# Performance work log

Measured on AMD Instinct MI355X. Metric: run time of the kernel, lower is better.

## Reference

```python
import jax, jax.numpy as jnp
import numpy as np

MASK_PROPORTION = 0.5
NEG_BIG = -99999999.0


def setup_inputs() -> dict:
    key = jax.random.key(0)
    k_x, k_w1, k_b1, k_w2, k_b2 = jax.random.split(key, 5)
    B, T, D, H = 32, 4096, 1024, 256
    x = jax.random.normal(k_x, (B, T, D), dtype=jnp.float32)
    s1 = 1.0 / np.sqrt(D)
    s2 = 1.0 / np.sqrt(H)
    W1 = jax.random.uniform(k_w1, (D, H), minval=-s1, maxval=s1, dtype=jnp.float32)
    b1 = jax.random.uniform(k_b1, (H,), minval=-s1, maxval=s1, dtype=jnp.float32)
    W2 = jax.random.uniform(k_w2, (H, 1), minval=-s2, maxval=s2, dtype=jnp.float32)
    b2 = jax.random.uniform(k_b2, (1,), minval=-s2, maxval=s2, dtype=jnp.float32)
    return {"x": x, "W1": W1, "b1": b1, "W2": W2, "b2": b2}


def reference(x, W1, b1, W2, b2):
    # e: [B, T, 1] attention scores from small MLP
    h = jnp.tanh(jnp.einsum("btd,dh->bth", x, W1) + b1)
    e = jnp.einsum("bth,ho->bto", h, W2) + b2  # [B, T, 1]

    T = e.shape[1]
    threshold_index = int(T * MASK_PROPORTION)
    sorted_e = jnp.sort(e, axis=1)
    threshold_value = sorted_e[:, threshold_index]          # [B, 1]
    # mask: +1 where e < threshold (kept), NEG_BIG where e >= threshold
    mask = jnp.where(e >= threshold_value[:, None, :], NEG_BIG, 1.0)
    e = e + mask
    beta = jax.nn.softmax(e, axis=1)                        # [B, T, 1]
    # bmm(beta^T, x) -> [B, 1, D], permute -> [B, D, 1], unsqueeze -> [B, D, 1, 1]
    out = jnp.einsum("bto,btd->bd", beta, x)
    return out[:, :, None, None]
```

## Files before the change

kernel.cpp:

```cpp
#include <hip/hip_runtime.h>
#include <hip/hip_bf16.h>
#include <math.h>

#define B_   32
#define T_   4096
#define D_   1024
#define H_   256
#define KTH  2048
#define NC   16
#define TC   (T_/NC)
#define BM   128
#define BKE  32
#define NTE  (D_/BKE)
#define EPSB 4.0e-3f
#define MAXBAND 256
#define RB   4

typedef __attribute__((ext_vector_type(8))) short short8;
typedef __attribute__((ext_vector_type(4))) float f32x4;

__device__ inline unsigned f2s(float f) {
    unsigned u = __float_as_uint(f);
    return (u & 0x80000000u) ? ~u : (u | 0x80000000u);
}
__device__ inline float s2f(unsigned s) {
    unsigned x = (s & 0x80000000u) ? (s & 0x7fffffffu) : ~s;
    return __uint_as_float(x);
}
__device__ inline unsigned f2bf_rne(float f) {
    unsigned u = __float_as_uint(f);
    return (u + 0x7FFFu + ((u >> 16) & 1u)) >> 16;
}
__device__ inline unsigned pk2(float a, float b) {
    return f2bf_rne(a) | (f2bf_rne(b) << 16);
}
__device__ inline int block_sum_i(int v, int* sb, int tid) {
    #pragma unroll
    for (int o = 32; o; o >>= 1) v += __shfl_down(v, o);
    __syncthreads();
    if ((tid & 63) == 0) sb[tid >> 6] = v;
    __syncthreads();
    return sb[0] + sb[1] + sb[2] + sb[3];
}
__device__ inline float block_max_f(float v, float* sb, int tid) {
    #pragma unroll
    for (int o = 32; o; o >>= 1) v = fmaxf(v, __shfl_down(v, o));
    __syncthreads();
    if ((tid & 63) == 0) sb[tid >> 6] = v;
    __syncthreads();
    return fmaxf(fmaxf(sb[0], sb[1]), fmaxf(sb[2], sb[3]));
}
__device__ inline float block_sum_f(float v, float* sb, int tid) {
    #pragma unroll
    for (int o = 32; o; o >>= 1) v += __shfl_down(v, o);
    __syncthreads();
    if ((tid & 63) == 0) sb[tid >> 6] = v;
    __syncthreads();
    return sb[0] + sb[1] + sb[2] + sb[3];
}

__global__ __launch_bounds__(256) void k_w1t(const float* __restrict__ W1,
                                             ushort* __restrict__ Whi) {
    __shared__ float tile[32][33];
    const int kb = blockIdx.x * 32, nb = blockIdx.y * 32;
    const int tx = threadIdx.x & 31, ty = threadIdx.x >> 5;
    #pragma unroll
    for (int i = 0; i < 4; i++)
        tile[ty + 8*i][tx] = W1[(long)(kb + ty + 8*i) * H_ + nb + tx];
    __syncthreads();
    #pragma unroll
    for (int i = 0; i < 4; i++) {
        long o = (long)(nb + ty + 8*i) * D_ + kb + tx;
        Whi[o] = (ushort)f2bf_rne(tile[tx][ty + 8*i]);
    }
}

__global__ __launch_bounds__(512, 4) void k_e_mfma(
    const float* __restrict__ x,
    const ushort* __restrict__ Whi,
    const float* __restrict__ b1, const float* __restrict__ W2,
    const float* __restrict__ b2, float* __restrict__ e_out)
{
    __shared__ ushort sA[2][BM * BKE];
    __shared__ ushort sB[2][H_ * BKE];
    __shared__ float  sRed[4][BM];

    const int tid  = threadIdx.x;
    const int lane = tid & 63;
    const int wv   = tid >> 6;
    const int wm   = wv >> 2, wn = wv & 3;
    const int l15  = lane & 15, lg = lane >> 4;
    const long row0 = (long)blockIdx.x * BM;

    const int ar = tid >> 2, aj = tid & 3;
    const float* aga = x + (row0 + ar) * (long)D_ + aj * 8;
    const int awo = (ar >> 4) * 512 + aj * 128 + (ar & 15) * 8;

    int  bn[2], bk[2], bdst[2];
    #pragma unroll
    for (int l = 0; l < 2; l++) {
        const int c = tid + l * 512;
        bn[l]   = (c >> 6) * 16 + (c & 15);
        bk[l]   = (c >> 4) & 3;
        bdst[l] = c * 8;
    }
    const ushort* bga0 = Whi + (long)bn[0] * D_ + bk[0] * 8;
    const ushort* bga1 = Whi + (long)bn[1] * D_ + bk[1] * 8;

    int aoff[4], boff[4];
    #pragma unroll
    for (int fm = 0; fm < 4; fm++) {
        const int slab = wm * 4 + fm;
        aoff[fm] = slab * 512 + lg * 128 + l15 * 8;
    }
    #pragma unroll
    for (int fn = 0; fn < 4; fn++) {
        const int slab = wn * 4 + fn;
        boff[fn] = slab * 512 + lg * 128 + l15 * 8;
    }

    f32x4 acc[4][4];
    #pragma unroll
    for (int i = 0; i < 4; i++)
        #pragma unroll
        for (int j = 0; j < 4; j++) acc[i][j] = (f32x4){0.f, 0.f, 0.f, 0.f};

    {
        float4 a0 = *(const float4*)(aga);
        float4 a1 = *(const float4*)(aga + 4);
        __builtin_amdgcn_global_load_lds(
            (const __attribute__((address_space(1))) unsigned int*)(bga0),
            (__attribute__((address_space(3))) unsigned int*)&sB[0][bdst[0]], 16, 0, 0);
        __builtin_amdgcn_global_load_lds(
            (const __attribute__((address_space(1))) unsigned int*)(bga1),
            (__attribute__((address_space(3))) unsigned int*)&sB[0][bdst[1]], 16, 0, 0);
        uint4 ap = make_uint4(pk2(a0.x, a0.y), pk2(a0.z, a0.w),
                              pk2(a1.x, a1.y), pk2(a1.z, a1.w));
        *(uint4*)&sA[0][awo] = ap;
    }
    __syncthreads();

    int cur = 0;
    for (int t = 0; t < NTE - 1; ++t) {
        const int ko = (t + 1) * BKE;
        float4 a0 = *(const float4*)(aga + ko);
        float4 a1 = *(const float4*)(aga + ko + 4);
        __builtin_amdgcn_global_load_lds(
            (const __attribute__((address_space(1))) unsigned int*)(bga0 + ko),
            (__attribute__((address_space(3))) unsigned int*)&sB[cur ^ 1][bdst[0]], 16, 0, 0);
        __builtin_amdgcn_global_load_lds(
            (const __attribute__((address_space(1))) unsigned int*)(bga1 + ko),
            (__attribute__((address_space(3))) unsigned int*)&sB[cur ^ 1][bdst[1]], 16, 0, 0);

        short8 bfr[4];
        #pragma unroll
        for (int fn = 0; fn < 4; fn++)
            bfr[fn] = *(const short8*)&sB[cur][boff[fn]];
        #pragma unroll
        for (int fm = 0; fm < 4; fm++) {
            short8 afr = *(const short8*)&sA[cur][aoff[fm]];
            #pragma unroll
            for (int fn = 0; fn < 4; fn++)
                acc[fm][fn] = __builtin_amdgcn_mfma_f32_16x16x32_bf16(afr, bfr[fn], acc[fm][fn], 0, 0, 0);
        }

        uint4 ap = make_uint4(pk2(a0.x, a0.y), pk2(a0.z, a0.w),
                              pk2(a1.x, a1.y), pk2(a1.z, a1.w));
        *(uint4*)&sA[cur ^ 1][awo] = ap;

        __syncthreads();
        cur ^= 1;
    }
    {
        short8 bfr[4];
        #pragma unroll
        for (int fn = 0; fn < 4; fn++)
            bfr[fn] = *(const short8*)&sB[cur][boff[fn]];
        #pragma unroll
        for (int fm = 0; fm < 4; fm++) {
            short8 afr = *(const short8*)&sA[cur][aoff[fm]];
            #pragma unroll
            for (int fn = 0; fn < 4; fn++)
                acc[fm][fn] = __builtin_amdgcn_mfma_f32_16x16x32_bf16(afr, bfr[fn], acc[fm][fn], 0, 0, 0);
        }
    }

    float b1v[4], w2v[4];
    #pragma unroll
    for (int fn = 0; fn < 4; fn++) {
        int j = wn * 64 + fn * 16 + l15;
        b1v[fn] = b1[j]; w2v[fn] = W2[j];
    }
    #pragma unroll
    for (int fm = 0; fm < 4; fm++) {
        #pragma unroll
        for (int r = 0; r < 4; r++) {
            float s = 0.f;
            #pragma unroll
            for (int fn = 0; fn < 4; fn++)
                s += tanhf(acc[fm][fn][r] + b1v[fn]) * w2v[fn];
            s += __shfl_xor(s, 1); s += __shfl_xor(s, 2);
            s += __shfl_xor(s, 4); s += __shfl_xor(s, 8);
            if (l15 == 0) sRed[wn][wm * 64 + fm * 16 + lg * 4 + r] = s;
        }
    }
    __syncthreads();
    if (tid < BM)
        e_out[row0 + tid] = sRed[0][tid] + sRed[1][tid] + sRed[2][tid] + sRed[3][tid] + b2[0];
}

template<int BUILD>
__global__ __launch_bounds__(256) void k_thresh(const float* __restrict__ e,
                                                float* __restrict__ beta,
                                                int* __restrict__ counts,
                                                int* __restrict__ list) {
    __shared__ int   sbi[4];
    __shared__ float sbf[4];
    __shared__ int   scnt;
    const int b = blockIdx.x, tid = threadIdx.x;
    const float* eb = e + (long)b * T_;

    float fe[16]; unsigned ue[16];
    #pragma unroll
    for (int i = 0; i < 16; i++) { fe[i] = eb[tid + i * 256]; ue[i] = f2s(fe[i]); }

    unsigned lo = 0u, hi = 0xFFFFFFFFu;
    while (lo < hi) {
        unsigned mid = lo + ((hi - lo) >> 1);
        int c = 0;
        #pragma unroll
        for (int i = 0; i < 16; i++) c += (ue[i] <= mid) ? 1 : 0;
        int total = block_sum_i(c, sbi, tid);
        if (total >= KTH + 1) hi = mid; else lo = mid + 1;
    }
    const float thr = s2f(lo);

    if (BUILD) {
        if (tid == 0) scnt = 0;
        __syncthreads();
        #pragma unroll
        for (int i = 0; i < 16; i++) {
            if (fabsf(fe[i] - thr) <= EPSB) {
                int p = atomicAdd(&scnt, 1);
                if (p < MAXBAND) list[b * MAXBAND + p] = tid + i * 256;
            }
        }
        __syncthreads();
        if (tid == 0) counts[b] = scnt < MAXBAND ? scnt : MAXBAND;
    } else {
        float m = -INFINITY;
        #pragma unroll
        for (int i = 0; i < 16; i++) if (fe[i] < thr) m = fmaxf(m, fe[i]);
        m = block_max_f(m, sbf, tid);
        float s = 0.f;
        #pragma unroll
        for (int i = 0; i < 16; i++) if (fe[i] < thr) s += expf(fe[i] - m);
        s = block_sum_f(s, sbf, tid);
        const float inv = 1.0f / s;
        #pragma unroll
        for (int i = 0; i < 16; i++)
            beta[(long)b * T_ + tid + i * 256] = (fe[i] < thr) ? expf(fe[i] - m) * inv : 0.0f;
    }
}

__global__ __launch_bounds__(256) void k_refine(const float* __restrict__ x,
        const float* __restrict__ W1, const float* __restrict__ b1,
        const float* __restrict__ W2, const float* __restrict__ b2,
        const int* __restrict__ counts, const int* __restrict__ list,
        float* __restrict__ e) {
    const int b   = blockIdx.y;
    const int blk = blockIdx.x;
    const int cnt = counts[b];
    const int tid = threadIdx.x;
    __shared__ float xs[RB][D_];
    __shared__ float sbf[4];

    for (int g = blk * RB; g < cnt; g += 16 * RB) {
        const int nr = min(RB, cnt - g);
        for (int j = 0; j < nr; j++) {
            const int t = list[b * MAXBAND + g + j];
            *(float4*)&xs[j][tid * 4] =
                *(const float4*)&x[((long)b * T_ + t) * D_ + tid * 4];
        }
        __syncthreads();

        float a0 = 0.f, a1 = 0.f, a2 = 0.f, a3 = 0.f;
        for (int k0 = 0; k0 < D_; k0 += 4) {
            const float w0 = W1[(long)(k0 + 0) * H_ + tid];
            const float w1v = W1[(long)(k0 + 1) * H_ + tid];
            const float w2q = W1[(long)(k0 + 2) * H_ + tid];
            const float w3 = W1[(long)(k0 + 3) * H_ + tid];
            {
                float4 xv = *(const float4*)&xs[0][k0];
                a0 = fmaf(xv.x, w0, a0); a0 = fmaf(xv.y, w1v, a0);
                a0 = fmaf(xv.z, w2q, a0); a0 = fmaf(xv.w, w3, a0);
            }
            {
                float4 xv = *(const float4*)&xs[1][k0];
                a1 = fmaf(xv.x, w0, a1); a1 = fmaf(xv.y, w1v, a1);
                a1 = fmaf(xv.z, w2q, a1); a1 = fmaf(xv.w, w3, a1);
            }
            {
                float4 xv = *(const float4*)&xs[2][k0];
                a2 = fmaf(xv.x, w0, a2); a2 = fmaf(xv.y, w1v, a2);
                a2 = fmaf(xv.z, w2q, a2); a2 = fmaf(xv.w, w3, a2);
            }
            {
                float4 xv = *(const float4*)&xs[3][k0];
                a3 = fmaf(xv.x, w0, a3); a3 = fmaf(xv.y, w1v, a3);
                a3 = fmaf(xv.z, w2q, a3); a3 = fmaf(xv.w, w3, a3);
            }
        }

        float aj[RB] = {a0, a1, a2, a3};
        for (int j = 0; j < nr; j++) {
            float v = tanhf(aj[j] + b1[tid]) * W2[tid];
            float tot = block_sum_f(v, sbf, tid);
            if (tid == 0) {
                const int t = list[b * MAXBAND + g + j];
                e[(long)b * T_ + t] = tot + b2[0];
            }
            __syncthreads();
        }
        __syncthreads();
    }
}

__global__ __launch_bounds__(256) void k_pv(const float* __restrict__ x,
                                            const float* __restrict__ beta,
                                            float* __restrict__ partial) {
    const int c = blockIdx.x, b = blockIdx.y, tid = threadIdx.x;
    __shared__ float sBeta[TC];
    sBeta[tid] = beta[(long)b * T_ + c * TC + tid];
    __syncthreads();
    float4 acc = {0.f, 0.f, 0.f, 0.f};
    const float* xb = x + ((long)b * T_ + (long)c * TC) * D_ + tid * 4;
    for (int t = 0; t < TC; t++) {
        float w = sBeta[t];
        if (w != 0.0f) {
            float4 v = *reinterpret_cast<const float4*>(xb + (long)t * D_);
            acc.x = fmaf(w, v.x, acc.x);
            acc.y = fmaf(w, v.y, acc.y);
            acc.z = fmaf(w, v.z, acc.z);
            acc.w = fmaf(w, v.w, acc.w);
        }
    }
    *reinterpret_cast<float4*>(&partial[(((long)b * NC) + c) * D_ + tid * 4]) = acc;
}

__global__ __launch_bounds__(256) void k_red(const float* __restrict__ partial,
                                             float* __restrict__ out) {
    const int b = blockIdx.x, tid = threadIdx.x;
    float4 acc = {0.f, 0.f, 0.f, 0.f};
    #pragma unroll
    for (int c = 0; c < NC; c++) {
        float4 v = *reinterpret_cast<const float4*>(&partial[(((long)b * NC) + c) * D_ + tid * 4]);
        acc.x += v.x; acc.y += v.y; acc.z += v.z; acc.w += v.w;
    }
    *reinterpret_cast<float4*>(&out[(long)b * D_ + tid * 4]) = acc;
}

extern "C" void kernel_launch(void* const* d_in, const int* in_sizes, int n_in,
                              void* d_out, int out_size, void* d_ws, size_t ws_size,
                              hipStream_t stream) {
    const float* x  = (const float*)d_in[0];
    const float* W1 = (const float*)d_in[1];
    const float* b1 = (const float*)d_in[2];
    const float* W2 = (const float*)d_in[3];
    const float* b2 = (const float*)d_in[4];
    float* out = (float*)d_out;

    char* ws = (char*)d_ws;
    float* e       = (float*)ws;  ws += (size_t)B_ * T_ * 4;
    float* beta    = (float*)ws;  ws += (size_t)B_ * T_ * 4;
    float* partial = (float*)ws;  ws += (size_t)B_ * NC * D_ * 4;
    ushort* Whi    = (ushort*)ws; ws += (size_t)H_ * D_ * 2;
    int* counts    = (int*)ws;    ws += 128;
    int* list      = (int*)ws;

    k_w1t<<<dim3(D_ / 32, H_ / 32), 256, 0, stream>>>(W1, Whi);
    k_e_mfma<<<(B_ * T_) / BM, 512, 0, stream>>>(x, Whi, b1, W2, b2, e);
    k_thresh<1><<<B_, 256, 0, stream>>>(e, nullptr, counts, list);
    k_refine<<<dim3(16, B_), 256, 0, stream>>>(x, W1, b1, W2, b2, counts, list, e);
    k_thresh<0><<<B_, 256, 0, stream>>>(e, beta, counts, list);
    k_pv<<<dim3(NC, B_), 256, 0, stream>>>(x, beta, partial);
    k_red<<<B_, 256, 0, stream>>>(partial, out);
}
```

Baseline: 353.3 us.

## Triple-buffer W1 tiles in MFMA GEMM and compact kept rows for weighted sum

```diff
diff --git a/kernel.cpp b/kernel.cpp
--- a/kernel.cpp
+++ b/kernel.cpp
@@ -7,17 +7,26 @@
 #define D_   1024
 #define H_   256
 #define KTH  2048
-#define NC   16
-#define TC   (T_/NC)
+#define SC   32
 #define BM   128
 #define BKE  32
 #define NTE  (D_/BKE)
+#define ABUF (BM*BKE)
+#define BBUF (H_*BKE)
 #define EPSB 4.0e-3f
 #define MAXBAND 256
 #define RB   4
 
 typedef __attribute__((ext_vector_type(8))) short short8;
 typedef __attribute__((ext_vector_type(4))) float f32x4;
+
+#define FENCE4() asm volatile("s_waitcnt vmcnt(4) lgkmcnt(0)" ::: "memory")
+#define FENCE0() asm volatile("s_waitcnt vmcnt(0) lgkmcnt(0)" ::: "memory")
+#define BARRIER() __builtin_amdgcn_s_barrier()
+#define SCHED()  __builtin_amdgcn_sched_barrier(0)
+#define GLL(src, dst) __builtin_amdgcn_global_load_lds( \
+    (const __attribute__((address_space(1))) unsigned int*)(src), \
+    (__attribute__((address_space(3))) unsigned int*)(dst), 16, 0, 0)
 
 __device__ inline unsigned f2s(float f) {
     unsigned u = __float_as_uint(f);
@@ -81,8 +90,8 @@
     const float* __restrict__ b1, const float* __restrict__ W2,
     const float* __restrict__ b2, float* __restrict__ e_out)
 {
-    __shared__ ushort sA[2][BM * BKE];
-    __shared__ ushort sB[2][H_ * BKE];
+    __shared__ ushort sA[2][ABUF];
+    __shared__ ushort sB[3][BBUF];
     __shared__ float  sRed[4][BM];
 
     const int tid  = threadIdx.x;
@@ -96,28 +105,20 @@
     const float* aga = x + (row0 + ar) * (long)D_ + aj * 8;
     const int awo = (ar >> 4) * 512 + aj * 128 + (ar & 15) * 8;
 
-    int  bn[2], bk[2], bdst[2];
-    #pragma unroll
-    for (int l = 0; l < 2; l++) {
-        const int c = tid + l * 512;
-        bn[l]   = (c >> 6) * 16 + (c & 15);
-        bk[l]   = (c >> 4) & 3;
-        bdst[l] = c * 8;
-    }
-    const ushort* bga0 = Whi + (long)bn[0] * D_ + bk[0] * 8;
-    const ushort* bga1 = Whi + (long)bn[1] * D_ + bk[1] * 8;
+    const int c0 = tid, c1 = tid + 512;
+    const int bn0 = (c0 >> 6) * 16 + (c0 & 15), bk0 = (c0 >> 4) & 3;
+    const int bn1 = (c1 >> 6) * 16 + (c1 & 15), bk1 = (c1 >> 4) & 3;
+    const ushort* bga0 = Whi + (long)bn0 * D_ + bk0 * 8;
+    const ushort* bga1 = Whi + (long)bn1 * D_ + bk1 * 8;
+    const int bdst0 = c0 * 8, bdst1 = c1 * 8;
 
     int aoff[4], boff[4];
     #pragma unroll
-    for (int fm = 0; fm < 4; fm++) {
-        const int slab = wm * 4 + fm;
-        aoff[fm] = slab * 512 + lg * 128 + l15 * 8;
-    }
-    #pragma unroll
-    for (int fn = 0; fn < 4; fn++) {
-        const int slab = wn * 4 + fn;
-        boff[fn] = slab * 512 + lg * 128 + l15 * 8;
-    }
+    for (int fm = 0; fm < 4; fm++)
+        aoff[fm] = (wm * 4 + fm) * 512 + lg * 128 + l15 * 8;
+    #pragma unroll
+    for (int fn = 0; fn < 4; fn++)
+        boff[fn] = (wn * 4 + fn) * 512 + lg * 128 + l15 * 8;
 
     f32x4 acc[4][4];
     #pragma unroll
@@ -125,65 +126,63 @@
         #pragma unroll
         for (int j = 0; j < 4; j++) acc[i][j] = (f32x4){0.f, 0.f, 0.f, 0.f};
 
-    {
-        float4 a0 = *(const float4*)(aga);
-        float4 a1 = *(const float4*)(aga + 4);
-        __builtin_amdgcn_global_load_lds(
-            (const __attribute__((address_space(1))) unsigned int*)(bga0),
-            (__attribute__((address_space(3))) unsigned int*)&sB[0][bdst[0]], 16, 0, 0);
-        __builtin_amdgcn_global_load_lds(
-            (const __attribute__((address_space(1))) unsigned int*)(bga1),
-            (__attribute__((address_space(3))) unsigned int*)&sB[0][bdst[1]], 16, 0, 0);
+    ushort* sBb = (ushort*)sB;
+    auto stageB = [&](int ko, int bi) {
+        GLL(bga0 + ko, sBb + bi * BBUF + bdst0);
+        GLL(bga1 + ko, sBb + bi * BBUF + bdst1);
+    };
+    auto writeA = [&](ushort* dst, const float4& a0, const float4& a1) {
         uint4 ap = make_uint4(pk2(a0.x, a0.y), pk2(a0.z, a0.w),
                               pk2(a1.x, a1.y), pk2(a1.z, a1.w));
-        *(uint4*)&sA[0][awo] = ap;
-    }
-    __syncthreads();
-
-    int cur = 0;
-    for (int t = 0; t < NTE - 1; ++t) {
-        const int ko = (t + 1) * BKE;
-        float4 a0 = *(const float4*)(aga + ko);
-        float4 a1 = *(const float4*)(aga + ko + 4);
-        __builtin_amdgcn_global_load_lds(
-            (const __attribute__((address_space(1))) unsigned int*)(bga0 + ko),
-            (__attribute__((address_space(3))) unsigned int*)&sB[cur ^ 1][bdst[0]], 16, 0, 0);
-        __builtin_amdgcn_global_load_lds(
-            (const __attribute__((address_space(1))) unsigned int*)(bga1 + ko),
-            (__attribute__((address_space(3))) unsigned int*)&sB[cur ^ 1][bdst[1]], 16, 0, 0);
-
+        *(uint4*)&dst[awo] = ap;
+    };
+    auto compute = [&](const ushort* sa, const ushort* sb) {
         short8 bfr[4];
         #pragma unroll
         for (int fn = 0; fn < 4; fn++)
-            bfr[fn] = *(const short8*)&sB[cur][boff[fn]];
+            bfr[fn] = *(const short8*)&sb[boff[fn]];
         #pragma unroll
         for (int fm = 0; fm < 4; fm++) {
-            short8 afr = *(const short8*)&sA[cur][aoff[fm]];
+            short8 afr = *(const short8*)&sa[aoff[fm]];
             #pragma unroll
             for (int fn = 0; fn < 4; fn++)
                 acc[fm][fn] = __builtin_amdgcn_mfma_f32_16x16x32_bf16(afr, bfr[fn], acc[fm][fn], 0, 0, 0);
         }
-
-        uint4 ap = make_uint4(pk2(a0.x, a0.y), pk2(a0.z, a0.w),
-                              pk2(a1.x, a1.y), pk2(a1.z, a1.w));
-        *(uint4*)&sA[cur ^ 1][awo] = ap;
-
-        __syncthreads();
-        cur ^= 1;
-    }
-    {
-        short8 bfr[4];
-        #pragma unroll
-        for (int fn = 0; fn < 4; fn++)
-            bfr[fn] = *(const short8*)&sB[cur][boff[fn]];
-        #pragma unroll
-        for (int fm = 0; fm < 4; fm++) {
-            short8 afr = *(const short8*)&sA[cur][aoff[fm]];
-            #pragma unroll
-            for (int fn = 0; fn < 4; fn++)
-                acc[fm][fn] = __builtin_amdgcn_mfma_f32_16x16x32_bf16(afr, bfr[fn], acc[fm][fn], 0, 0, 0);
-        }
-    }
+    };
+
+    float4 rA0a = *(const float4*)(aga);
+    float4 rA0b = *(const float4*)(aga + 4);
+    stageB(0, 0);
+    float4 rA1a = *(const float4*)(aga + BKE);
+    float4 rA1b = *(const float4*)(aga + BKE + 4);
+    stageB(BKE, 1);
+    writeA(sA[0], rA0a, rA0b);
+
+    for (int t = 0; t < NTE - 2; t += 2) {
+        FENCE4(); BARRIER(); SCHED();
+        {
+            const int ko = (t + 2) * BKE;
+            rA0a = *(const float4*)(aga + ko);
+            rA0b = *(const float4*)(aga + ko + 4);
+            stageB(ko, (t + 2) % 3);
+            compute(sA[0], sBb + (t % 3) * BBUF);
+            writeA(sA[1], rA1a, rA1b);
+        }
+        FENCE4(); BARRIER(); SCHED();
+        {
+            const int ko = (t + 3) * BKE;
+            rA1a = *(const float4*)(aga + ko);
+            rA1b = *(const float4*)(aga + ko + 4);
+            stageB(ko, (t + 3) % 3);
+            compute(sA[1], sBb + ((t + 1) % 3) * BBUF);
+            writeA(sA[0], rA0a, rA0b);
+        }
+    }
+    FENCE4(); BARRIER(); SCHED();
+    compute(sA[0], sBb + ((NTE - 2) % 3) * BBUF);
+    writeA(sA[1], rA1a, rA1b);
+    FENCE0(); BARRIER(); SCHED();
+    compute(sA[1], sBb + ((NTE - 1) % 3) * BBUF);
 
     float b1v[4], w2v[4];
     #pragma unroll
@@ -211,18 +210,28 @@
 
 template<int BUILD>
 __global__ __launch_bounds__(256) void k_thresh(const float* __restrict__ e,
-                                                float* __restrict__ beta,
                                                 int* __restrict__ counts,
-                                                int* __restrict__ list) {
+                                                int* __restrict__ list,
+                                                int* __restrict__ sidx,
+                                                float* __restrict__ sval,
+                                                int* __restrict__ scount) {
     __shared__ int   sbi[4];
     __shared__ float sbf[4];
+    __shared__ int   wsum[4];
     __shared__ int   scnt;
     const int b = blockIdx.x, tid = threadIdx.x;
+    const int lane = tid & 63, wid = tid >> 6;
     const float* eb = e + (long)b * T_;
+    const int t0 = tid * 16;
 
     float fe[16]; unsigned ue[16];
     #pragma unroll
-    for (int i = 0; i < 16; i++) { fe[i] = eb[tid + i * 256]; ue[i] = f2s(fe[i]); }
+    for (int i = 0; i < 16; i += 4) {
+        float4 v = *(const float4*)(eb + t0 + i);
+        fe[i] = v.x; fe[i+1] = v.y; fe[i+2] = v.z; fe[i+3] = v.w;
+    }
+    #pragma unroll
+    for (int i = 0; i < 16; i++) ue[i] = f2s(fe[i]);
 
     unsigned lo = 0u, hi = 0xFFFFFFFFu;
     while (lo < hi) {
@@ -242,7 +251,7 @@
         for (int i = 0; i < 16; i++) {
             if (fabsf(fe[i] - thr) <= EPSB) {
                 int p = atomicAdd(&scnt, 1);
-                if (p < MAXBAND) list[b * MAXBAND + p] = tid + i * 256;
+                if (p < MAXBAND) list[b * MAXBAND + p] = t0 + i;
             }
         }
         __syncthreads();
@@ -257,9 +266,31 @@
         for (int i = 0; i < 16; i++) if (fe[i] < thr) s += expf(fe[i] - m);
         s = block_sum_f(s, sbf, tid);
         const float inv = 1.0f / s;
-        #pragma unroll
-        for (int i = 0; i < 16; i++)
-            beta[(long)b * T_ + tid + i * 256] = (fe[i] < thr) ? expf(fe[i] - m) * inv : 0.0f;
+
+        int c = 0;
+        #pragma unroll
+        for (int i = 0; i < 16; i++) c += (fe[i] < thr) ? 1 : 0;
+        int p = c;
+        #pragma unroll
+        for (int o = 1; o < 64; o <<= 1) {
+            int y = __shfl_up(p, o);
+            if (lane >= o) p += y;
+        }
+        if (lane == 63) wsum[wid] = p;
+        __syncthreads();
+        int base = 0;
+        #pragma unroll
+        for (int w = 0; w < 4; w++) base += (w < wid) ? wsum[w] : 0;
+        int pos = base + p - c;
+        #pragma unroll
+        for (int i = 0; i < 16; i++) {
+            if (fe[i] < thr) {
+                sidx[(long)b * T_ + pos] = t0 + i;
+                sval[(long)b * T_ + pos] = expf(fe[i] - m) * inv;
+                pos++;
+            }
+        }
+        if (tid == 0) scount[b] = wsum[0] + wsum[1] + wsum[2] + wsum[3];
     }
 }
 
@@ -327,25 +358,34 @@
 }
 
 __global__ __launch_bounds__(256) void k_pv(const float* __restrict__ x,
-                                            const float* __restrict__ beta,
+                                            const int* __restrict__ sidx,
+                                            const float* __restrict__ sval,
+                                            const int* __restrict__ scount,
                                             float* __restrict__ partial) {
     const int c = blockIdx.x, b = blockIdx.y, tid = threadIdx.x;
-    __shared__ float sBeta[TC];
-    sBeta[tid] = beta[(long)b * T_ + c * TC + tid];
-    __syncthreads();
+    const int cnt = scount[b];
+    const int len = (cnt + SC - 1) / SC;
+    const int k0 = c * len;
+    const int nl = min(len, cnt - k0);
+    __shared__ int   si[96];
+    __shared__ float sv[96];
+    if (tid < nl) {
+        si[tid] = sidx[(long)b * T_ + k0 + tid];
+        sv[tid] = sval[(long)b * T_ + k0 + tid];
+    }
+    __syncthreads();
+
     float4 acc = {0.f, 0.f, 0.f, 0.f};
-    const float* xb = x + ((long)b * T_ + (long)c * TC) * D_ + tid * 4;
-    for (int t = 0; t < TC; t++) {
-        float w = sBeta[t];
-        if (w != 0.0f) {
-            float4 v = *reinterpret_cast<const float4*>(xb + (long)t * D_);
-            acc.x = fmaf(w, v.x, acc.x);
-            acc.y = fmaf(w, v.y, acc.y);
-            acc.z = fmaf(w, v.z, acc.z);
-            acc.w = fmaf(w, v.w, acc.w);
-        }
-    }
-    *reinterpret_cast<float4*>(&partial[(((long)b * NC) + c) * D_ + tid * 4]) = acc;
+    const float* xb = x + (long)b * T_ * D_ + tid * 4;
+    for (int k = 0; k < nl; k++) {
+        const float w = sv[k];
+        float4 v = *(const float4*)(xb + (long)si[k] * D_);
+        acc.x = fmaf(w, v.x, acc.x);
+        acc.y = fmaf(w, v.y, acc.y);
+        acc.z = fmaf(w, v.z, acc.z);
+        acc.w = fmaf(w, v.w, acc.w);
+    }
+    *(float4*)&partial[(((long)b * SC) + c) * D_ + tid * 4] = acc;
 }
 
 __global__ __launch_bounds__(256) void k_red(const float* __restrict__ partial,
@@ -353,11 +393,11 @@
     const int b = blockIdx.x, tid = threadIdx.x;
     float4 acc = {0.f, 0.f, 0.f, 0.f};
     #pragma unroll
-    for (int c = 0; c < NC; c++) {
-        float4 v = *reinterpret_cast<const float4*>(&partial[(((long)b * NC) + c) * D_ + tid * 4]);
+    for (int c = 0; c < SC; c++) {
+        float4 v = *(const float4*)&partial[(((long)b * SC) + c) * D_ + tid * 4];
         acc.x += v.x; acc.y += v.y; acc.z += v.z; acc.w += v.w;
     }
-    *reinterpret_cast<float4*>(&out[(long)b * D_ + tid * 4]) = acc;
+    *(float4*)&out[(long)b * D_ + tid * 4] = acc;
 }
 
 extern "C" void kernel_launch(void* const* d_in, const int* in_sizes, int n_in,
@@ -372,17 +412,19 @@
 
     char* ws = (char*)d_ws;
     float* e       = (float*)ws;  ws += (size_t)B_ * T_ * 4;
-    float* beta    = (float*)ws;  ws += (size_t)B_ * T_ * 4;
-    float* partial = (float*)ws;  ws += (size_t)B_ * NC * D_ * 4;
+    int*   sidx    = (int*)ws;    ws += (size_t)B_ * T_ * 4;
+    float* sval    = (float*)ws;  ws += (size_t)B_ * T_ * 4;
+    float* partial = (float*)ws;  ws += (size_t)B_ * SC * D_ * 4;
     ushort* Whi    = (ushort*)ws; ws += (size_t)H_ * D_ * 2;
     int* counts    = (int*)ws;    ws += 128;
+    int* scountp   = (int*)ws;    ws += 128;
     int* list      = (int*)ws;
 
     k_w1t<<<dim3(D_ / 32, H_ / 32), 256, 0, stream>>>(W1, Whi);
     k_e_mfma<<<(B_ * T_) / BM, 512, 0, stream>>>(x, Whi, b1, W2, b2, e);
-    k_thresh<1><<<B_, 256, 0, stream>>>(e, nullptr, counts, list);
+    k_thresh<1><<<B_, 256, 0, stream>>>(e, counts, list, sidx, sval, scountp);
     k_refine<<<dim3(16, B_), 256, 0, stream>>>(x, W1, b1, W2, b2, counts, list, e);
-    k_thresh<0><<<B_, 256, 0, stream>>>(e, beta, counts, list);
-    k_pv<<<dim3(NC, B_), 256, 0, stream>>>(x, beta, partial);
+    k_thresh<0><<<B_, 256, 0, stream>>>(e, counts, list, sidx, sval, scountp);
+    k_pv<<<dim3(SC, B_), 256, 0, stream>>>(x, sidx, sval, scountp, partial);
     k_red<<<B_, 256, 0, stream>>>(partial, out);
 }
```

Measured after the change: 319.2 us. -9.7%, faster.
